# Kernel optimization log

Measured on AMD Instinct MI355X. Metric: run time of the kernel, lower is better.

Reference implementation:

```python
import jax, jax.numpy as jnp
import numpy as np

N_NODES = 100000
N_EDGES = 1600000
D_IN = 128
D_OUT = 128
NEG_SLOPE = 0.01  # torch F.leaky_relu default


def setup_inputs() -> dict:
    key = jax.random.key(0)
    k1, k2, k3, k4, k5 = jax.random.split(key, 5)
    h = jax.random.normal(k1, (N_NODES, D_IN), dtype=jnp.float32)
    # nn.Linear default init scale ~ 1/sqrt(fan_in)
    W = jax.random.normal(k2, (D_IN, D_OUT), dtype=jnp.float32) / np.sqrt(D_IN)
    attn_w = jax.random.normal(k3, (2 * D_OUT,), dtype=jnp.float32) / np.sqrt(2 * D_OUT)
    edge_src = jax.random.randint(k4, (N_EDGES,), 0, N_NODES, dtype=jnp.int32)
    edge_dst = jax.random.randint(k5, (N_EDGES,), 0, N_NODES, dtype=jnp.int32)
    return {"h": h, "W": W, "attn_w": attn_w, "edge_src": edge_src, "edge_dst": edge_dst}


def reference(h, W, attn_w, edge_src, edge_dst):
    n = h.shape[0]
    d = W.shape[1]
    z = h @ W                                   # [N, d]
    # attention_func(cat([z_src, z_dst])) == z_src @ a[:d] + z_dst @ a[d:]
    s_src = z @ attn_w[:d]                      # [N]
    s_dst = z @ attn_w[d:]                      # [N]
    e = jax.nn.leaky_relu(s_src[edge_src] + s_dst[edge_dst], NEG_SLOPE)  # [E]
    # segment softmax over incoming edges of each dst node
    m = jax.ops.segment_max(e, edge_dst, num_segments=n)   # [N], -inf for empty
    ex = jnp.exp(e - m[edge_dst])                           # [E]
    denom = jax.ops.segment_sum(ex, edge_dst, num_segments=n)  # [N]
    alpha = ex / denom[edge_dst]                             # [E]
    # weighted neighbor sum: sum_j alpha_ij * z_j
    out = jax.ops.segment_sum(alpha[:, None] * z[edge_src], edge_dst, num_segments=n)
    return out
```

## Files before the change

### kernel.cpp

```cpp
#include <hip/hip_runtime.h>

#define D 128
#define NEG_SLOPE 0.01f
#define BSHIFT 7
#define B1 1024
#define STR 136
#define SCHUNK 4096
#define SLOT 2560

typedef __attribute__((ext_vector_type(8))) short short8;
typedef __attribute__((ext_vector_type(4))) float floatx4;

__device__ __forceinline__ unsigned f2bf_rne(float x) {
    unsigned u = __float_as_uint(x);
    return (u + 0x7fffu + ((u >> 16) & 1u)) >> 16;
}
#define BF_LO(u) __uint_as_float((u) << 16)
#define BF_HI(u) __uint_as_float((u) & 0xffff0000u)

__global__ void init_gcur(int* __restrict__ gcur) {
    const int i = threadIdx.x;
    gcur[i] = i * SLOT;
}

__global__ __launch_bounds__(1024) void sort_scatter(const int* __restrict__ esrc,
                                                     const int* __restrict__ edst,
                                                     int* __restrict__ gcur,
                                                     int* __restrict__ pairs, int E) {
    __shared__ int cnt[B1], exc[B1], gbs[B1], cur[B1];
    __shared__ int spk[SCHUNK];
    __shared__ unsigned short sbkt[SCHUNK];
    const int t = threadIdx.x;
    cnt[t] = 0; cur[t] = 0;
    __syncthreads();

    const int e0 = blockIdx.x * SCHUNK;
    const int n  = min(SCHUNK, E - e0);

    int pk[4], bk[4];
#pragma unroll
    for (int k = 0; k < 4; ++k) {
        const int i = t + k * 1024;
        if (i < n) {
            const int d = edst[e0 + i];
            const int s = esrc[e0 + i];
            bk[k] = d >> BSHIFT;
            pk[k] = (s << BSHIFT) | (d & 127);
            atomicAdd(&cnt[bk[k]], 1);
        } else {
            bk[k] = -1;
        }
    }
    __syncthreads();

    exc[t] = cnt[t];
    __syncthreads();
    for (int off = 1; off < B1; off <<= 1) {
        int v = (t >= off) ? exc[t - off] : 0;
        __syncthreads();
        exc[t] += v;
        __syncthreads();
    }
    const int myexc = exc[t] - cnt[t];
    exc[t] = myexc;
    if (cnt[t] > 0) gbs[t] = atomicAdd(&gcur[t], cnt[t]);
    __syncthreads();

#pragma unroll
    for (int k = 0; k < 4; ++k) {
        if (bk[k] >= 0) {
            const int p = exc[bk[k]] + atomicAdd(&cur[bk[k]], 1);
            spk[p]  = pk[k];
            sbkt[p] = (unsigned short)bk[k];
        }
    }
    __syncthreads();

    for (int i = t; i < n; i += 1024) {
        const int b = sbkt[i];
        const int pos = gbs[b] + (i - exc[b]);
        if (pos < (b + 1) * SLOT) pairs[pos] = spk[i];
    }
}

__global__ __launch_bounds__(256) void fine_build(const int* __restrict__ pairs,
                                                  const int* __restrict__ gcur,
                                                  int* __restrict__ beg,
                                                  int* __restrict__ ncnt,
                                                  int* __restrict__ adj, int N) {
    __shared__ int cnt[128], sc[128], cur[128];
    const int b = blockIdx.x;
    const int base = b << BSHIFT;
    const int nd = min(128, N - base);
    const int t = threadIdx.x;
    const int s0 = b * SLOT;
    const int e1 = min(gcur[b], s0 + SLOT);
    if (t < 128) { cnt[t] = 0; cur[t] = 0; }
    __syncthreads();
    for (int i = s0 + t; i < e1; i += 256)
        atomicAdd(&cnt[pairs[i] & 127], 1);
    __syncthreads();
    if (t < 128) sc[t] = cnt[t];
    __syncthreads();
    for (int off = 1; off < 128; off <<= 1) {
        int v = (t < 128 && t >= off) ? sc[t - off] : 0;
        __syncthreads();
        if (t < 128) sc[t] += v;
        __syncthreads();
    }
    if (t < nd) {
        beg[base + t]  = s0 + sc[t] - cnt[t];
        ncnt[base + t] = cnt[t];
    }
    __syncthreads();
    for (int i = s0 + t; i < e1; i += 256) {
        const int pkv = pairs[i];
        const int d = pkv & 127;
        const int pos = s0 + (sc[d] - cnt[d]) + atomicAdd(&cur[d], 1);
        adj[pos] = pkv >> BSHIFT;
    }
}

__global__ __launch_bounds__(256) void gemm_zs(const float* __restrict__ h,
                                               const float* __restrict__ W,
                                               const float* __restrict__ aw,
                                               unsigned short* __restrict__ z,
                                               float* __restrict__ s_src,
                                               float* __restrict__ s_dst,
                                               int N, int ntiles) {
    __shared__ unsigned short ws_hi[D * STR];
    __shared__ unsigned short ws_lo[D * STR];
    const int t = threadIdx.x;
    for (int i = t; i < D * D; i += 256) {
        int k = i >> 7, n = i & 127;
        float x = W[i];
        unsigned hi = f2bf_rne(x);
        float hf = __uint_as_float(hi << 16);
        unsigned lo = __float_as_uint(x - hf) >> 16;
        ws_hi[n * STR + k] = (unsigned short)hi;
        ws_lo[n * STR + k] = (unsigned short)lo;
    }
    __syncthreads();

    const int lane = t & 63, quad = lane >> 4, l16 = lane & 15;

    for (int tile = blockIdx.x; tile < ntiles; tile += gridDim.x) {
        const int rowbase = tile * 64 + (t >> 6) * 16;
        const int arow = min(rowbase + l16, N - 1);
        const float* __restrict__ hrow = h + (size_t)arow * D;

        floatx4 acc[8];
#pragma unroll
        for (int ct = 0; ct < 8; ++ct) acc[ct] = (floatx4){0.f, 0.f, 0.f, 0.f};

#pragma unroll
        for (int kk = 0; kk < 4; ++kk) {
            const int k0 = kk * 32 + quad * 8;
            float4 x0 = *(const float4*)&hrow[k0];
            float4 x1 = *(const float4*)&hrow[k0 + 4];
            float xs[8] = {x0.x, x0.y, x0.z, x0.w, x1.x, x1.y, x1.z, x1.w};
            union { short8 v; unsigned short u[8]; } ahi, alo;
#pragma unroll
            for (int i = 0; i < 8; ++i) {
                unsigned hi = f2bf_rne(xs[i]);
                float hf = __uint_as_float(hi << 16);
                ahi.u[i] = (unsigned short)hi;
                alo.u[i] = (unsigned short)(__float_as_uint(xs[i] - hf) >> 16);
            }
#pragma unroll
            for (int ct = 0; ct < 8; ++ct) {
                const int bo = (ct * 16 + l16) * STR + k0;
                short8 bhi = *(const short8*)&ws_hi[bo];
                short8 blo = *(const short8*)&ws_lo[bo];
                acc[ct] = __builtin_amdgcn_mfma_f32_16x16x32_bf16(ahi.v, bhi, acc[ct], 0, 0, 0);
                acc[ct] = __builtin_amdgcn_mfma_f32_16x16x32_bf16(alo.v, bhi, acc[ct], 0, 0, 0);
                acc[ct] = __builtin_amdgcn_mfma_f32_16x16x32_bf16(ahi.v, blo, acc[ct], 0, 0, 0);
            }
        }

#pragma unroll
        for (int ct = 0; ct < 8; ++ct)
#pragma unroll
            for (int reg = 0; reg < 4; ++reg) {
                int r = rowbase + quad * 4 + reg;
                if (r < N)
                    z[(size_t)r * D + ct * 16 + l16] = (unsigned short)f2bf_rne(acc[ct][reg]);
            }

        float ps[4] = {0.f, 0.f, 0.f, 0.f}, pd[4] = {0.f, 0.f, 0.f, 0.f};
#pragma unroll
        for (int ct = 0; ct < 8; ++ct) {
            float as = aw[ct * 16 + l16];
            float ad = aw[128 + ct * 16 + l16];
#pragma unroll
            for (int reg = 0; reg < 4; ++reg) {
                ps[reg] = fmaf(acc[ct][reg], as, ps[reg]);
                pd[reg] = fmaf(acc[ct][reg], ad, pd[reg]);
            }
        }
#pragma unroll
        for (int reg = 0; reg < 4; ++reg)
#pragma unroll
            for (int o = 1; o < 16; o <<= 1) {
                ps[reg] += __shfl_xor(ps[reg], o, 64);
                pd[reg] += __shfl_xor(pd[reg], o, 64);
            }
        if (l16 == 0) {
#pragma unroll
            for (int reg = 0; reg < 4; ++reg) {
                int r = rowbase + quad * 4 + reg;
                if (r < N) { s_src[r] = ps[reg]; s_dst[r] = pd[reg]; }
            }
        }
    }
}

__global__ __launch_bounds__(256) void aggregate(const unsigned short* __restrict__ z,
                                                 const float* __restrict__ s_src,
                                                 const float* __restrict__ s_dst,
                                                 const int* __restrict__ beg_,
                                                 const int* __restrict__ ncnt_,
                                                 const int* __restrict__ adj,
                                                 float* __restrict__ out, int N) {
    const int lane = threadIdx.x & 63;
    const int half = lane >> 5;
    const int l32  = lane & 31;
    const int q2   = l32 >> 4;
    const int l16  = lane & 15;
    const int hb   = half << 5;
    const int pairBase = blockIdx.x * 8 + (threadIdx.x >> 6) * 2;
    if (pairBase >= N) return;
    const int nodeA = pairBase, nodeB = pairBase + 1;
    const int cA = ncnt_[nodeA], bA = beg_[nodeA];
    int cB = 0, bB = 0;
    if (nodeB < N) { cB = ncnt_[nodeB]; bB = beg_[nodeB]; }

    auto fma8 = [&](float* ac, float w, const uint4& v) {
        ac[0] = fmaf(w, BF_LO(v.x), ac[0]); ac[1] = fmaf(w, BF_HI(v.x), ac[1]);
        ac[2] = fmaf(w, BF_LO(v.y), ac[2]); ac[3] = fmaf(w, BF_HI(v.y), ac[3]);
        ac[4] = fmaf(w, BF_LO(v.z), ac[4]); ac[5] = fmaf(w, BF_HI(v.z), ac[5]);
        ac[6] = fmaf(w, BF_LO(v.w), ac[6]); ac[7] = fmaf(w, BF_HI(v.w), ac[7]);
    };

    if (max(cA, cB) <= 32) {
        const int myn = pairBase + half;
        const int mb  = half ? bB : bA;
        const int mc  = half ? cB : cA;
        const float sd = s_dst[myn < N ? myn : 0];
        int s = 0; float e = -INFINITY;
        if (l32 < mc) {
            s = adj[mb + l32];
            float tt = s_src[s] + sd;
            e = (tt >= 0.f) ? tt : NEG_SLOPE * tt;
        }
        int sj[4]; uint4 zv[4];
#pragma unroll
        for (int u = 0; u < 4; ++u) sj[u] = __shfl(s, hb + u * 2 + q2, 64);
#pragma unroll
        for (int u = 0; u < 4; ++u)
            zv[u] = *(const uint4*)&z[(size_t)sj[u] * D + l16 * 8];

        float mx = e;
#pragma unroll
        for (int o = 16; o; o >>= 1) mx = fmaxf(mx, __shfl_xor(mx, o, 64));
        float ex = (l32 < mc) ? __expf(e - mx) : 0.f;
        float sum = ex;
#pragma unroll
        for (int o = 16; o; o >>= 1) sum += __shfl_xor(sum, o, 64);
        const float inv = (mc > 0) ? 1.f / sum : 0.f;
        const float w = ex * inv;

        float a[8] = {0.f,0.f,0.f,0.f,0.f,0.f,0.f,0.f};
        float bacc[8] = {0.f,0.f,0.f,0.f,0.f,0.f,0.f,0.f};
#pragma unroll
        for (int u = 0; u < 4; ++u) {
            const int ji = u * 2 + q2;
            float wj = __shfl(w, hb + ji, 64);
            wj = (ji < mc) ? wj : 0.f;
            fma8((u & 1) ? bacc : a, wj, zv[u]);
        }
        for (int jj = 8; jj < mc; jj += 8) {
            int ji2[4]; float wj[4]; int sj2[4];
#pragma unroll
            for (int u = 0; u < 4; ++u) {
                ji2[u] = jj + u * 2 + q2;
                wj[u]  = __shfl(w, hb + ji2[u], 64);
                sj2[u] = __shfl(s, hb + ji2[u], 64);
                wj[u]  = (ji2[u] < mc) ? wj[u] : 0.f;
            }
            uint4 z0 = *(const uint4*)&z[(size_t)sj2[0] * D + l16 * 8];
            uint4 z1 = *(const uint4*)&z[(size_t)sj2[1] * D + l16 * 8];
            uint4 z2 = *(const uint4*)&z[(size_t)sj2[2] * D + l16 * 8];
            uint4 z3 = *(const uint4*)&z[(size_t)sj2[3] * D + l16 * 8];
            fma8(a, wj[0], z0);
            fma8(bacc, wj[1], z1);
            fma8(a, wj[2], z2);
            fma8(bacc, wj[3], z3);
        }
#pragma unroll
        for (int i = 0; i < 8; ++i) {
            a[i] += bacc[i];
            a[i] += __shfl_xor(a[i], 16, 64);
        }
        if (q2 == 0 && myn < N) {
            float* o = &out[(size_t)myn * D + l16 * 8];
            *(float4*)o       = make_float4(a[0], a[1], a[2], a[3]);
            *(float4*)(o + 4) = make_float4(a[4], a[5], a[6], a[7]);
        }
        return;
    }

    const int q = lane >> 4;
    for (int which = 0; which < 2; ++which) {
        const int myn = which ? nodeB : nodeA;
        if (myn >= N) break;
        const int mb = which ? bB : bA;
        const int mc = which ? cB : cA;
        const float sd = s_dst[myn];
        float a[8] = {0.f,0.f,0.f,0.f,0.f,0.f,0.f,0.f};
        float bacc[8] = {0.f,0.f,0.f,0.f,0.f,0.f,0.f,0.f};
        float mx = -INFINITY;
        for (int j = lane; j < mc; j += 64) {
            float tt = s_src[adj[mb + j]] + sd;
            tt = (tt >= 0.f) ? tt : NEG_SLOPE * tt;
            mx = fmaxf(mx, tt);
        }
#pragma unroll
        for (int o = 32; o; o >>= 1) mx = fmaxf(mx, __shfl_xor(mx, o, 64));
        float sum = 0.f;
        for (int j = lane; j < mc; j += 64) {
            float tt = s_src[adj[mb + j]] + sd;
            tt = (tt >= 0.f) ? tt : NEG_SLOPE * tt;
            sum += __expf(tt - mx);
        }
#pragma unroll
        for (int o = 32; o; o >>= 1) sum += __shfl_xor(sum, o, 64);
        const float inv = (mc > 0) ? 1.f / sum : 0.f;
        for (int base2 = 0; base2 < mc; base2 += 64) {
            const int cc = min(64, mc - base2);
            int s = 0; float w = 0.f;
            if (lane < cc) {
                s = adj[mb + base2 + lane];
                float tt = s_src[s] + sd;
                tt = (tt >= 0.f) ? tt : NEG_SLOPE * tt;
                w = __expf(tt - mx) * inv;
            }
            for (int jj = 0; jj < cc; jj += 8) {
                const int ja = jj + q;
                const int jb = ja + 4;
                float wa = __shfl(w, ja, 64); int sa = __shfl(s, ja, 64);
                float wb = __shfl(w, jb, 64); int sb = __shfl(s, jb, 64);
                wa = (ja < cc) ? wa : 0.f;
                wb = (jb < cc) ? wb : 0.f;
                uint4 za = *(const uint4*)&z[(size_t)sa * D + l16 * 8];
                uint4 zb = *(const uint4*)&z[(size_t)sb * D + l16 * 8];
                fma8(a, wa, za);
                fma8(bacc, wb, zb);
            }
        }
#pragma unroll
        for (int i = 0; i < 8; ++i) {
            a[i] += bacc[i];
            a[i] += __shfl_xor(a[i], 16, 64);
            a[i] += __shfl_xor(a[i], 32, 64);
        }
        if (q == 0) {
            float* o = &out[(size_t)myn * D + l16 * 8];
            *(float4*)o       = make_float4(a[0], a[1], a[2], a[3]);
            *(float4*)(o + 4) = make_float4(a[4], a[5], a[6], a[7]);
        }
    }
}

extern "C" void kernel_launch(void* const* d_in, const int* in_sizes, int n_in,
                              void* d_out, int out_size, void* d_ws, size_t ws_size,
                              hipStream_t stream) {
    const float* h    = (const float*)d_in[0];
    const float* W    = (const float*)d_in[1];
    const float* aw   = (const float*)d_in[2];
    const int*   esrc = (const int*)d_in[3];
    const int*   edst = (const int*)d_in[4];
    float* out = (float*)d_out;

    const int N = in_sizes[0] / D;
    const int E = in_sizes[3];
    const int NB1    = (N + 127) >> BSHIFT;
    const int NSORT  = (E + SCHUNK - 1) / SCHUNK;
    const int NTILES = (N + 63) / 64;
    const int NGEMM  = min(NTILES, 521);

    char* p = (char*)d_ws;
    auto carve = [&](size_t bytes) {
        void* r = (void*)p;
        p += (bytes + 255) & ~size_t(255);
        return r;
    };
    unsigned short* z = (unsigned short*)carve(size_t(N) * D * sizeof(unsigned short));
    float* s_src  = (float*)carve(size_t(N) * sizeof(float));
    float* s_dst  = (float*)carve(size_t(N) * sizeof(float));
    int*   pairs  = (int*)carve(size_t(NB1) * SLOT * sizeof(int));
    int*   adj    = (int*)carve(size_t(NB1) * SLOT * sizeof(int));
    int*   beg    = (int*)carve(size_t(N) * sizeof(int));
    int*   ncnt   = (int*)carve(size_t(N) * sizeof(int));
    int*   gcur   = (int*)carve(size_t(B1) * sizeof(int));
    (void)ws_size; (void)n_in; (void)out_size;

    init_gcur<<<1, B1, 0, stream>>>(gcur);
    sort_scatter<<<NSORT, 1024, 0, stream>>>(esrc, edst, gcur, pairs, E);
    fine_build<<<NB1, 256, 0, stream>>>(pairs, gcur, beg, ncnt, adj, N);
    gemm_zs<<<NGEMM, 256, 0, stream>>>(h, W, aw, z, s_src, s_dst, N, NTILES);
    aggregate<<<(N + 7) / 8, 256, 0, stream>>>(z, s_src, s_dst, beg, ncnt, adj, out, N);
}
```

Measured before the change: 247.3 us.

## Precompute W bf16 hi/lo MFMA fragments and drop LDS staging in GEMM

A new small kernel converts W into bf16 hi/lo split fragments laid out in MFMA operand order and stores them in global workspace. The GEMM kernel now loads those fragments straight from global memory (L2-resident) instead of having each block convert W into a 68KB LDS tile, and launches one block per 64-row tile instead of a persistent grid. This removes per-block conversion and the large LDS footprint, which allows higher occupancy. The cost is an extra kernel launch and B-operand reads through the cache on every k-step.

```diff
diff --git a/kernel.cpp b/kernel.cpp
--- a/kernel.cpp
+++ b/kernel.cpp
@@ -4,7 +4,6 @@
 #define NEG_SLOPE 0.01f
 #define BSHIFT 7
 #define B1 1024
-#define STR 136
 #define SCHUNK 4096
 #define SLOT 2560
 
@@ -21,6 +20,23 @@
 __global__ void init_gcur(int* __restrict__ gcur) {
     const int i = threadIdx.x;
     gcur[i] = i * SLOT;
+}
+
+__global__ __launch_bounds__(256) void prep_wfrag(const float* __restrict__ W,
+                                                  unsigned short* __restrict__ whi,
+                                                  unsigned short* __restrict__ wlo) {
+    const int idx = blockIdx.x * 256 + threadIdx.x;
+    const int j    = idx & 7;
+    const int lane = (idx >> 3) & 63;
+    const int tk   = idx >> 9;
+    const int kk = tk & 3, ct = tk >> 2;
+    const int k = kk * 32 + (lane >> 4) * 8 + j;
+    const int n = ct * 16 + (lane & 15);
+    const float x = W[k * D + n];
+    const unsigned hi = f2bf_rne(x);
+    const float hf = __uint_as_float(hi << 16);
+    whi[idx] = (unsigned short)hi;
+    wlo[idx] = (unsigned short)(__float_as_uint(x - hf) >> 16);
 }
 
 __global__ __launch_bounds__(1024) void sort_scatter(const int* __restrict__ esrc,
@@ -122,95 +138,79 @@
 }
 
 __global__ __launch_bounds__(256) void gemm_zs(const float* __restrict__ h,
-                                               const float* __restrict__ W,
+                                               const unsigned short* __restrict__ whi,
+                                               const unsigned short* __restrict__ wlo,
                                                const float* __restrict__ aw,
                                                unsigned short* __restrict__ z,
                                                float* __restrict__ s_src,
-                                               float* __restrict__ s_dst,
-                                               int N, int ntiles) {
-    __shared__ unsigned short ws_hi[D * STR];
-    __shared__ unsigned short ws_lo[D * STR];
+                                               float* __restrict__ s_dst, int N) {
     const int t = threadIdx.x;
-    for (int i = t; i < D * D; i += 256) {
-        int k = i >> 7, n = i & 127;
-        float x = W[i];
-        unsigned hi = f2bf_rne(x);
-        float hf = __uint_as_float(hi << 16);
-        unsigned lo = __float_as_uint(x - hf) >> 16;
-        ws_hi[n * STR + k] = (unsigned short)hi;
-        ws_lo[n * STR + k] = (unsigned short)lo;
-    }
-    __syncthreads();
-
     const int lane = t & 63, quad = lane >> 4, l16 = lane & 15;
-
-    for (int tile = blockIdx.x; tile < ntiles; tile += gridDim.x) {
-        const int rowbase = tile * 64 + (t >> 6) * 16;
-        const int arow = min(rowbase + l16, N - 1);
-        const float* __restrict__ hrow = h + (size_t)arow * D;
-
-        floatx4 acc[8];
-#pragma unroll
-        for (int ct = 0; ct < 8; ++ct) acc[ct] = (floatx4){0.f, 0.f, 0.f, 0.f};
-
-#pragma unroll
-        for (int kk = 0; kk < 4; ++kk) {
-            const int k0 = kk * 32 + quad * 8;
-            float4 x0 = *(const float4*)&hrow[k0];
-            float4 x1 = *(const float4*)&hrow[k0 + 4];
-            float xs[8] = {x0.x, x0.y, x0.z, x0.w, x1.x, x1.y, x1.z, x1.w};
-            union { short8 v; unsigned short u[8]; } ahi, alo;
-#pragma unroll
-            for (int i = 0; i < 8; ++i) {
-                unsigned hi = f2bf_rne(xs[i]);
-                float hf = __uint_as_float(hi << 16);
-                ahi.u[i] = (unsigned short)hi;
-                alo.u[i] = (unsigned short)(__float_as_uint(xs[i] - hf) >> 16);
-            }
-#pragma unroll
-            for (int ct = 0; ct < 8; ++ct) {
-                const int bo = (ct * 16 + l16) * STR + k0;
-                short8 bhi = *(const short8*)&ws_hi[bo];
-                short8 blo = *(const short8*)&ws_lo[bo];
-                acc[ct] = __builtin_amdgcn_mfma_f32_16x16x32_bf16(ahi.v, bhi, acc[ct], 0, 0, 0);
-                acc[ct] = __builtin_amdgcn_mfma_f32_16x16x32_bf16(alo.v, bhi, acc[ct], 0, 0, 0);
-                acc[ct] = __builtin_amdgcn_mfma_f32_16x16x32_bf16(ahi.v, blo, acc[ct], 0, 0, 0);
-            }
-        }
-
-#pragma unroll
-        for (int ct = 0; ct < 8; ++ct)
-#pragma unroll
-            for (int reg = 0; reg < 4; ++reg) {
-                int r = rowbase + quad * 4 + reg;
-                if (r < N)
-                    z[(size_t)r * D + ct * 16 + l16] = (unsigned short)f2bf_rne(acc[ct][reg]);
-            }
-
-        float ps[4] = {0.f, 0.f, 0.f, 0.f}, pd[4] = {0.f, 0.f, 0.f, 0.f};
+    const int rowbase = blockIdx.x * 64 + (t >> 6) * 16;
+    const int arow = min(rowbase + l16, N - 1);
+    const float* __restrict__ hrow = h + (size_t)arow * D;
+
+    floatx4 acc[8];
+#pragma unroll
+    for (int ct = 0; ct < 8; ++ct) acc[ct] = (floatx4){0.f, 0.f, 0.f, 0.f};
+
+#pragma unroll
+    for (int kk = 0; kk < 4; ++kk) {
+        const int k0 = kk * 32 + quad * 8;
+        float4 x0 = *(const float4*)&hrow[k0];
+        float4 x1 = *(const float4*)&hrow[k0 + 4];
+        float xs[8] = {x0.x, x0.y, x0.z, x0.w, x1.x, x1.y, x1.z, x1.w};
+        union { short8 v; unsigned short u[8]; } ahi, alo;
+#pragma unroll
+        for (int i = 0; i < 8; ++i) {
+            unsigned hi = f2bf_rne(xs[i]);
+            float hf = __uint_as_float(hi << 16);
+            ahi.u[i] = (unsigned short)hi;
+            alo.u[i] = (unsigned short)(__float_as_uint(xs[i] - hf) >> 16);
+        }
 #pragma unroll
         for (int ct = 0; ct < 8; ++ct) {
-            float as = aw[ct * 16 + l16];
-            float ad = aw[128 + ct * 16 + l16];
-#pragma unroll
-            for (int reg = 0; reg < 4; ++reg) {
-                ps[reg] = fmaf(acc[ct][reg], as, ps[reg]);
-                pd[reg] = fmaf(acc[ct][reg], ad, pd[reg]);
-            }
-        }
-#pragma unroll
-        for (int reg = 0; reg < 4; ++reg)
-#pragma unroll
-            for (int o = 1; o < 16; o <<= 1) {
-                ps[reg] += __shfl_xor(ps[reg], o, 64);
-                pd[reg] += __shfl_xor(pd[reg], o, 64);
-            }
-        if (l16 == 0) {
-#pragma unroll
-            for (int reg = 0; reg < 4; ++reg) {
-                int r = rowbase + quad * 4 + reg;
-                if (r < N) { s_src[r] = ps[reg]; s_dst[r] = pd[reg]; }
-            }
+            const int fo = ((ct * 4 + kk) * 64 + lane) * 8;
+            short8 bhi = *(const short8*)&whi[fo];
+            short8 blo = *(const short8*)&wlo[fo];
+            acc[ct] = __builtin_amdgcn_mfma_f32_16x16x32_bf16(ahi.v, bhi, acc[ct], 0, 0, 0);
+            acc[ct] = __builtin_amdgcn_mfma_f32_16x16x32_bf16(alo.v, bhi, acc[ct], 0, 0, 0);
+            acc[ct] = __builtin_amdgcn_mfma_f32_16x16x32_bf16(ahi.v, blo, acc[ct], 0, 0, 0);
+        }
+    }
+
+#pragma unroll
+    for (int ct = 0; ct < 8; ++ct)
+#pragma unroll
+        for (int reg = 0; reg < 4; ++reg) {
+            int r = rowbase + quad * 4 + reg;
+            if (r < N)
+                z[(size_t)r * D + ct * 16 + l16] = (unsigned short)f2bf_rne(acc[ct][reg]);
+        }
+
+    float ps[4] = {0.f, 0.f, 0.f, 0.f}, pd[4] = {0.f, 0.f, 0.f, 0.f};
+#pragma unroll
+    for (int ct = 0; ct < 8; ++ct) {
+        float as = aw[ct * 16 + l16];
+        float ad = aw[128 + ct * 16 + l16];
+#pragma unroll
+        for (int reg = 0; reg < 4; ++reg) {
+            ps[reg] = fmaf(acc[ct][reg], as, ps[reg]);
+            pd[reg] = fmaf(acc[ct][reg], ad, pd[reg]);
+        }
+    }
+#pragma unroll
+    for (int reg = 0; reg < 4; ++reg)
+#pragma unroll
+        for (int o = 1; o < 16; o <<= 1) {
+            ps[reg] += __shfl_xor(ps[reg], o, 64);
+            pd[reg] += __shfl_xor(pd[reg], o, 64);
+        }
+    if (l16 == 0) {
+#pragma unroll
+        for (int reg = 0; reg < 4; ++reg) {
+            int r = rowbase + quad * 4 + reg;
+            if (r < N) { s_src[r] = ps[reg]; s_dst[r] = pd[reg]; }
         }
     }
 }
@@ -384,10 +384,8 @@
 
     const int N = in_sizes[0] / D;
     const int E = in_sizes[3];
-    const int NB1    = (N + 127) >> BSHIFT;
-    const int NSORT  = (E + SCHUNK - 1) / SCHUNK;
-    const int NTILES = (N + 63) / 64;
-    const int NGEMM  = min(NTILES, 521);
+    const int NB1   = (N + 127) >> BSHIFT;
+    const int NSORT = (E + SCHUNK - 1) / SCHUNK;
 
     char* p = (char*)d_ws;
     auto carve = [&](size_t bytes) {
@@ -403,11 +401,14 @@
     int*   beg    = (int*)carve(size_t(N) * sizeof(int));
     int*   ncnt   = (int*)carve(size_t(N) * sizeof(int));
     int*   gcur   = (int*)carve(size_t(B1) * sizeof(int));
+    unsigned short* whi = (unsigned short*)carve(16384 * sizeof(unsigned short));
+    unsigned short* wlo = (unsigned short*)carve(16384 * sizeof(unsigned short));
     (void)ws_size; (void)n_in; (void)out_size;
 
+    prep_wfrag<<<64, 256, 0, stream>>>(W, whi, wlo);
     init_gcur<<<1, B1, 0, stream>>>(gcur);
     sort_scatter<<<NSORT, 1024, 0, stream>>>(esrc, edst, gcur, pairs, E);
     fine_build<<<NB1, 256, 0, stream>>>(pairs, gcur, beg, ncnt, adj, N);
-    gemm_zs<<<NGEMM, 256, 0, stream>>>(h, W, aw, z, s_src, s_dst, N, NTILES);
+    gemm_zs<<<(N + 63) / 64, 256, 0, stream>>>(h, whi, wlo, aw, z, s_src, s_dst, N);
     aggregate<<<(N + 7) / 8, 256, 0, stream>>>(z, s_src, s_dst, beg, ncnt, adj, out, N);
 }
```

Result: faster. 222.4 us (-10.1%).
